# Kernel tuning notes

Hardware: AMD Instinct MI355X
Metric: run time of the kernel (lower is better)

## Reference

```python
import jax, jax.numpy as jnp
import numpy as np

N, P, S, M, K, L = 1024, 4, 12, 64, 16, 8
SNR = 20.0
PWR = 1.0
DECAY = L // 2  # Channel is built with decay = L // 2
MK = M + K
SMK = (S + 1) * MK
LOUT = L + SMK - 1  # full linear-convolution length


def _to_c(x):
    return x[..., 0] + 1j * x[..., 1]


def _to_r(x):
    return jnp.stack([x.real, x.imag], axis=-1)


def setup_inputs() -> dict:
    key = jax.random.key(0)
    k1, k2, k3, k4 = jax.random.split(key, 4)
    return {
        "x": jax.random.normal(k1, (N, P, S, M, 2), jnp.float32),
        "pilot_raw": jax.random.normal(k2, (N, P, 1, M, 2), jnp.float32),
        "cof_unit": jax.random.normal(k3, (N, P, L, 2), jnp.float32),
        "noise_unit": jax.random.normal(k4, (N, P, S + 1, MK, 2), jnp.float32),
    }


def reference(x, pilot_raw, cof_unit, noise_unit):
    # --- pilot: Normalize -> ifft -> add CP (done once in torch __init__) ---
    power = jnp.mean(pilot_raw ** 2, axis=(-2, -1), keepdims=True)  # (N,P,1,1,1)
    alpha = jnp.sqrt(PWR / 2) / jnp.sqrt(power)
    pilot = jnp.fft.ifft(_to_c(alpha * pilot_raw), axis=-1)          # (N,P,1,M) complex
    pilot = jnp.concatenate([pilot[..., -K:], pilot], axis=-1)        # add CP -> (N,P,1,MK)

    # --- payload: ifft -> add CP ---
    xt = jnp.fft.ifft(_to_c(x), axis=-1)                              # (N,P,S,M)
    xt = jnp.concatenate([xt[..., -K:], xt], axis=-1)                 # (N,P,S,MK)

    sig = jnp.concatenate([pilot, xt], axis=2).reshape(N, P, SMK)     # serialized complex signal

    # --- channel taps: sqrt(power_profile/2) * randn (cof is None path) ---
    prof = jnp.exp(-jnp.arange(L, dtype=jnp.float32) / DECAY)
    prof = prof / jnp.sum(prof)
    cof = _to_c(jnp.sqrt(prof / 2)[:, None] * cof_unit)               # (N,P,L) complex

    cof_true = jnp.concatenate([cof, jnp.zeros((N, P, M - L), cof.dtype)], axis=-1)
    H_true = jnp.fft.fft(cof_true, axis=-1)                           # (N,P,M)

    # --- L-tap linear convolution (equivalent to dense Toeplitz bmm) ---
    s_pad = jnp.pad(sig, ((0, 0), (0, 0), (L - 1, L - 1)))            # (N,P,SMK+2(L-1))
    y = jnp.zeros((N, P, LOUT), sig.dtype)
    for t in range(L):  # fixed small tap count
        y = y + cof[:, :, t:t + 1] * s_pad[:, :, L - 1 - t: L - 1 - t + LOUT]

    out = y[:, :, :SMK].reshape(N, P, S + 1, MK)

    # --- AWGN (default SNR path, isTest=False) ---
    noise_pwr = PWR / (M * 10.0 ** (0.1 * SNR))
    out = out + np.sqrt(noise_pwr / 2) * _to_c(noise_unit)

    # --- split pilot/signal, remove CP, FFT back to frequency domain ---
    info_pilot = jnp.fft.fft(out[:, :, 0:1, K:], axis=-1)             # (N,P,1,M)
    info_sig = jnp.fft.fft(out[:, :, 1:, K:], axis=-1)                # (N,P,S,M)

    return (_to_r(info_pilot), _to_r(info_sig), _to_r(H_true),
            jnp.float32(noise_pwr))
```

## Files before the change

kernel.cpp:

```cpp
#include <hip/hip_runtime.h>
#include <math.h>

#define NN   1024
#define PP   4
#define SS   12
#define MM   64
#define KK   16
#define LL   8
#define MKK  80
#define NSYM 13
#define SMK  1040
#define NITEMS 832

#define OFF_PILOT  0
#define OFF_SIG    524288
#define OFF_H      6815744
#define OFF_SCALAR 7340032

#define NOISE_PWR   1.5625e-4f
#define NOISE_SCALE 8.8388347648318447e-3f
#define TWO_SUM_PROF 7.8179726742f

__device__ __forceinline__ float2 shflx(float2 v, int mask) {
    return make_float2(__shfl_xor(v.x, mask), __shfl_xor(v.y, mask));
}

template<int DIR>
__device__ __forceinline__ float2 fft64(float2 v, const float2* tw, int lane) {
    #pragma unroll
    for (int s = 0; s < 6; ++s) {
        const int half = 32 >> s;
        float2 o = shflx(v, half);
        const bool up = (lane & half) != 0;
        float dx = up ? (o.x - v.x) : (o.x + v.x);
        float dy = up ? (o.y - v.y) : (o.y + v.y);
        float tx = tw[s].x;
        float ty = DIR ? -tw[s].y : tw[s].y;
        v.x = dx * tx - dy * ty;
        v.y = dx * ty + dy * tx;
    }
    return v;
}

__global__ __launch_bounds__(256) void ofdm_kernel(
    const float2* __restrict__ x,
    const float2* __restrict__ pilot_raw,
    const float2* __restrict__ cof_unit,
    const float2* __restrict__ noise_unit,
    float2* __restrict__ out_pilot,
    float2* __restrict__ out_sig,
    float2* __restrict__ out_H,
    float*  __restrict__ out_scalar)
{
    const int b    = blockIdx.x;
    const int tid  = threadIdx.x;
    const int wid  = tid >> 6;
    const int lane = tid & 63;

    __shared__ float2 sig[SMK];
    __shared__ float2 z[NITEMS];
    __shared__ float2 cofs[LL];

    const float2* xb = x          + (size_t)b * (SS*MM);
    const float2* pb = pilot_raw  + (size_t)b * MM;
    const float2* cb = cof_unit   + (size_t)b * LL;
    const float2* nb = noise_unit + (size_t)b * (NSYM*MKK);

    if (tid < LL) {
        float sc = sqrtf(__expf(-(float)tid * 0.25f) * (1.0f / TWO_SUM_PROF));
        float2 u = cb[tid];
        cofs[tid] = make_float2(sc * u.x, sc * u.y);
    }

    float2 twid[6];
    #pragma unroll
    for (int s = 0; s < 6; ++s) {
        const int half = 32 >> s;
        const int m = lane & (half - 1);
        float ang = -6.2831853071795864769f * (float)(m << s) * (1.0f / 64.0f);
        float sn, cs;
        __sincosf(ang, &sn, &cs);
        twid[s] = (lane & half) ? make_float2(cs, sn) : make_float2(1.0f, 0.0f);
    }

    const int rb = (int)(__brev((unsigned)lane) >> 26);

    float alpha = 0.0f;
    float2 pv = make_float2(0.f, 0.f);
    if (wid == 0) {
        pv = pb[lane];
        float ss = pv.x * pv.x + pv.y * pv.y;
        #pragma unroll
        for (int off = 32; off > 0; off >>= 1)
            ss += __shfl_xor(ss, off);
        alpha = sqrtf(64.0f / ss);
    }

    for (int sym = wid; sym < NSYM; sym += 4) {
        float2 v;
        if (sym == 0) v = make_float2(alpha * pv.x, alpha * pv.y);
        else          v = xb[(sym - 1) * MM + lane];
        v = fft64<1>(v, twid, lane);
        v.x *= (1.0f / 64.0f);
        v.y *= (1.0f / 64.0f);
        const int n = rb;
        sig[sym * MKK + KK + n] = v;
        if (n >= MM - KK) sig[sym * MKK + n - (MM - KK)] = v;
    }

    if (wid == 1) {
        float2 h = make_float2(0.f, 0.f);
        if (lane < LL) {
            float sc = sqrtf(__expf(-(float)lane * 0.25f) * (1.0f / TWO_SUM_PROF));
            float2 u = cb[lane];
            h = make_float2(sc * u.x, sc * u.y);
        }
        h = fft64<0>(h, twid, lane);
        out_H[(size_t)b * MM + rb] = h;
    }

    __syncthreads();

    for (int i = tid; i < NITEMS; i += 256) {
        const int s = i >> 6, m = i & 63;
        const int pos = s * MKK + KK + m;
        float2 acc = make_float2(0.f, 0.f);
        #pragma unroll
        for (int t = 0; t < LL; ++t) {
            float2 c = cofs[t];
            float2 v = sig[pos - t];
            acc.x += c.x * v.x - c.y * v.y;
            acc.y += c.x * v.y + c.y * v.x;
        }
        float2 nu = nb[pos];
        acc.x += NOISE_SCALE * nu.x;
        acc.y += NOISE_SCALE * nu.y;
        z[i] = acc;
    }

    __syncthreads();

    for (int sym = wid; sym < NSYM; sym += 4) {
        float2 v = z[sym * MM + lane];
        v = fft64<0>(v, twid, lane);
        if (sym == 0) out_pilot[(size_t)b * MM + rb] = v;
        else          out_sig[(size_t)b * (SS*MM) + (sym - 1) * MM + rb] = v;
    }

    if (b == 0 && tid == 0) out_scalar[0] = NOISE_PWR;
}

extern "C" void kernel_launch(void* const* d_in, const int* in_sizes, int n_in,
                              void* d_out, int out_size, void* d_ws, size_t ws_size,
                              hipStream_t stream) {
    const float2* x  = (const float2*)d_in[0];
    const float2* pr = (const float2*)d_in[1];
    const float2* cu = (const float2*)d_in[2];
    const float2* nu = (const float2*)d_in[3];

    float* out = (float*)d_out;
    float2* out_pilot = (float2*)(out + OFF_PILOT);
    float2* out_sig   = (float2*)(out + OFF_SIG);
    float2* out_H     = (float2*)(out + OFF_H);
    float*  out_sc    = out + OFF_SCALAR;

    ofdm_kernel<<<dim3(NN*PP), dim3(256), 0, stream>>>(
        x, pr, cu, nu, out_pilot, out_sig, out_H, out_sc);
}
```

Before: 127.8 us.

## Fuse FIR into bit-reversed-input DIT FFT and batch symbols per wavefront

Each wavefront now processes its three or four symbols at once, interleaving their shuffle-based FFTs to expose instruction-level parallelism. The forward FFT switches to decimation-in-time with bit-reversed input. This lets each lane compute the channel FIR plus noise directly at its bit-reversed position and feed it straight into the FFT, removing the z shared buffer and one __syncthreads. Channel taps are held in registers, and the H_true FFT is batched alongside the payload symbols. Outputs are now stored contiguously in natural order, at the cost of higher register pressure from the batched arrays.

After: 120.7 us. -5.5%, faster.

```diff
diff --git a/kernel.cpp b/kernel.cpp
--- a/kernel.cpp
+++ b/kernel.cpp
@@ -10,7 +10,6 @@
 #define MKK  80
 #define NSYM 13
 #define SMK  1040
-#define NITEMS 832
 
 #define OFF_PILOT  0
 #define OFF_SIG    524288
@@ -19,27 +18,52 @@
 
 #define NOISE_PWR   1.5625e-4f
 #define NOISE_SCALE 8.8388347648318447e-3f
-#define TWO_SUM_PROF 7.8179726742f
+#define INV_2SUM    0.1279105570f
 
 __device__ __forceinline__ float2 shflx(float2 v, int mask) {
     return make_float2(__shfl_xor(v.x, mask), __shfl_xor(v.y, mask));
 }
 
-template<int DIR>
-__device__ __forceinline__ float2 fft64(float2 v, const float2* tw, int lane) {
+
+template<int CONJ, int NS>
+__device__ __forceinline__ void fft64_dif(float2* v, const float2* tw, const float* sgn) {
+    #pragma unroll
+    for (int s = 5; s >= 0; --s) {
+        float2 o[NS];
+        #pragma unroll
+        for (int j = 0; j < NS; ++j) o[j] = shflx(v[j], 1 << s);
+        const float sg = sgn[s], tx = tw[s].x;
+        const float ty = CONJ ? -tw[s].y : tw[s].y;
+        #pragma unroll
+        for (int j = 0; j < NS; ++j) {
+            float dx = fmaf(sg, v[j].x, o[j].x);
+            float dy = fmaf(sg, v[j].y, o[j].y);
+            v[j].x = dx * tx - dy * ty;
+            v[j].y = dx * ty + dy * tx;
+        }
+    }
+}
+
+template<int NS>
+__device__ __forceinline__ void fft64_dit(float2* v, const float2* tw, const float* sgn) {
     #pragma unroll
     for (int s = 0; s < 6; ++s) {
-        const int half = 32 >> s;
-        float2 o = shflx(v, half);
-        const bool up = (lane & half) != 0;
-        float dx = up ? (o.x - v.x) : (o.x + v.x);
-        float dy = up ? (o.y - v.y) : (o.y + v.y);
-        float tx = tw[s].x;
-        float ty = DIR ? -tw[s].y : tw[s].y;
-        v.x = dx * tx - dy * ty;
-        v.y = dx * ty + dy * tx;
-    }
-    return v;
+        const float sg = sgn[s], tx = tw[s].x, ty = tw[s].y;
+        float ax[NS], ay[NS];
+        #pragma unroll
+        for (int j = 0; j < NS; ++j) {
+            ax[j] = v[j].x * tx - v[j].y * ty;
+            ay[j] = v[j].x * ty + v[j].y * tx;
+        }
+        float2 o[NS];
+        #pragma unroll
+        for (int j = 0; j < NS; ++j) o[j] = shflx(make_float2(ax[j], ay[j]), 1 << s);
+        #pragma unroll
+        for (int j = 0; j < NS; ++j) {
+            v[j].x = fmaf(sg, ax[j], o[j].x);
+            v[j].y = fmaf(sg, ay[j], o[j].y);
+        }
+    }
 }
 
 __global__ __launch_bounds__(256) void ofdm_kernel(
@@ -58,93 +82,120 @@
     const int lane = tid & 63;
 
     __shared__ float2 sig[SMK];
-    __shared__ float2 z[NITEMS];
-    __shared__ float2 cofs[LL];
 
     const float2* xb = x          + (size_t)b * (SS*MM);
     const float2* pb = pilot_raw  + (size_t)b * MM;
     const float2* cb = cof_unit   + (size_t)b * LL;
     const float2* nb = noise_unit + (size_t)b * (NSYM*MKK);
 
-    if (tid < LL) {
-        float sc = sqrtf(__expf(-(float)tid * 0.25f) * (1.0f / TWO_SUM_PROF));
-        float2 u = cb[tid];
-        cofs[tid] = make_float2(sc * u.x, sc * u.y);
-    }
-
-    float2 twid[6];
+    float2 tw[6];
+    float  sgn[6];
     #pragma unroll
     for (int s = 0; s < 6; ++s) {
-        const int half = 32 >> s;
-        const int m = lane & (half - 1);
-        float ang = -6.2831853071795864769f * (float)(m << s) * (1.0f / 64.0f);
+        const int h = 1 << s;
+        const bool up = (lane & h) != 0;
+        sgn[s] = up ? -1.0f : 1.0f;
+        float ang = -6.2831853071795864769f * (float)(lane & (h - 1)) / (float)(2 * h);
         float sn, cs;
         __sincosf(ang, &sn, &cs);
-        twid[s] = (lane & half) ? make_float2(cs, sn) : make_float2(1.0f, 0.0f);
-    }
-
+        tw[s] = up ? make_float2(cs, sn) : make_float2(1.0f, 0.0f);
+    }
     const int rb = (int)(__brev((unsigned)lane) >> 26);
 
-    float alpha = 0.0f;
-    float2 pv = make_float2(0.f, 0.f);
+    float2 cof[LL];
+    #pragma unroll
+    for (int t = 0; t < LL; ++t) {
+        float sc = sqrtf(__expf(-(float)t * 0.25f) * INV_2SUM);
+        float2 u = cb[t];
+        cof[t] = make_float2(sc * u.x, sc * u.y);
+    }
+
+    auto store_sig = [&](int sym, float2 vv) {
+        vv.x *= (1.0f / 64.0f);
+        vv.y *= (1.0f / 64.0f);
+        sig[sym * MKK + KK + rb] = vv;
+        if (rb >= MM - KK) sig[sym * MKK + rb - (MM - KK)] = vv;
+    };
+
     if (wid == 0) {
-        pv = pb[lane];
-        float ss = pv.x * pv.x + pv.y * pv.y;
+        float2 v[4];
+        float2 pv = pb[lane];
+        v[1] = xb[3 * MM + lane];
+        v[2] = xb[7 * MM + lane];
+        v[3] = xb[11 * MM + lane];
+        float ssq = pv.x * pv.x + pv.y * pv.y;
         #pragma unroll
         for (int off = 32; off > 0; off >>= 1)
-            ss += __shfl_xor(ss, off);
-        alpha = sqrtf(64.0f / ss);
-    }
-
-    for (int sym = wid; sym < NSYM; sym += 4) {
-        float2 v;
-        if (sym == 0) v = make_float2(alpha * pv.x, alpha * pv.y);
-        else          v = xb[(sym - 1) * MM + lane];
-        v = fft64<1>(v, twid, lane);
-        v.x *= (1.0f / 64.0f);
-        v.y *= (1.0f / 64.0f);
-        const int n = rb;
-        sig[sym * MKK + KK + n] = v;
-        if (n >= MM - KK) sig[sym * MKK + n - (MM - KK)] = v;
-    }
-
-    if (wid == 1) {
-        float2 h = make_float2(0.f, 0.f);
-        if (lane < LL) {
-            float sc = sqrtf(__expf(-(float)lane * 0.25f) * (1.0f / TWO_SUM_PROF));
-            float2 u = cb[lane];
-            h = make_float2(sc * u.x, sc * u.y);
-        }
-        h = fft64<0>(h, twid, lane);
-        out_H[(size_t)b * MM + rb] = h;
+            ssq += __shfl_xor(ssq, off);
+        float alpha = sqrtf(64.0f / ssq);
+        v[0] = make_float2(alpha * pv.x, alpha * pv.y);
+        fft64_dif<1, 4>(v, tw, sgn);
+        store_sig(0, v[0]); store_sig(4, v[1]); store_sig(8, v[2]); store_sig(12, v[3]);
+    } else {
+        float2 v[3];
+        v[0] = xb[(wid - 1) * MM + lane];
+        v[1] = xb[(wid + 3) * MM + lane];
+        v[2] = xb[(wid + 7) * MM + lane];
+        fft64_dif<1, 3>(v, tw, sgn);
+        store_sig(wid, v[0]); store_sig(wid + 4, v[1]); store_sig(wid + 8, v[2]);
     }
 
     __syncthreads();
 
-    for (int i = tid; i < NITEMS; i += 256) {
-        const int s = i >> 6, m = i & 63;
-        const int pos = s * MKK + KK + m;
-        float2 acc = make_float2(0.f, 0.f);
+    auto fir = [&](int sym) -> float2 {
+        const int pos = sym * MKK + KK + rb;
+        float2 nu = nb[pos];
+        float2 acc = make_float2(NOISE_SCALE * nu.x, NOISE_SCALE * nu.y);
         #pragma unroll
         for (int t = 0; t < LL; ++t) {
-            float2 c = cofs[t];
-            float2 v = sig[pos - t];
-            acc.x += c.x * v.x - c.y * v.y;
-            acc.y += c.x * v.y + c.y * v.x;
-        }
-        float2 nu = nb[pos];
-        acc.x += NOISE_SCALE * nu.x;
-        acc.y += NOISE_SCALE * nu.y;
-        z[i] = acc;
-    }
-
-    __syncthreads();
-
-    for (int sym = wid; sym < NSYM; sym += 4) {
-        float2 v = z[sym * MM + lane];
-        v = fft64<0>(v, twid, lane);
-        if (sym == 0) out_pilot[(size_t)b * MM + rb] = v;
-        else          out_sig[(size_t)b * (SS*MM) + (sym - 1) * MM + rb] = v;
+            float2 c = cof[t];
+            float2 s2 = sig[pos - t];
+            acc.x += c.x * s2.x - c.y * s2.y;
+            acc.y += c.x * s2.y + c.y * s2.x;
+        }
+        return acc;
+    };
+
+    const size_t ob = (size_t)b * MM;
+    const size_t osb = (size_t)b * (SS * MM);
+
+    if (wid <= 1) {
+        float2 v[4];
+        v[0] = fir(wid);
+        v[1] = fir(wid + 4);
+        v[2] = fir(wid + 8);
+        if (wid == 0) {
+            v[3] = fir(12);
+        } else {
+            float2 h = make_float2(0.0f, 0.0f);
+            if (rb < LL) {
+                float sc = sqrtf(__expf(-(float)rb * 0.25f) * INV_2SUM);
+                float2 u = cb[rb];
+                h = make_float2(sc * u.x, sc * u.y);
+            }
+            v[3] = h;
+        }
+        fft64_dit<4>(v, tw, sgn);
+        if (wid == 0) {
+            out_pilot[ob + lane]            = v[0];
+            out_sig[osb + 3 * MM + lane]    = v[1];
+            out_sig[osb + 7 * MM + lane]    = v[2];
+            out_sig[osb + 11 * MM + lane]   = v[3];
+        } else {
+            out_sig[osb + 0 * MM + lane]    = v[0];
+            out_sig[osb + 4 * MM + lane]    = v[1];
+            out_sig[osb + 8 * MM + lane]    = v[2];
+            out_H[ob + lane]                = v[3];
+        }
+    } else {
+        float2 v[3];
+        v[0] = fir(wid);
+        v[1] = fir(wid + 4);
+        v[2] = fir(wid + 8);
+        fft64_dit<3>(v, tw, sgn);
+        out_sig[osb + (wid - 1) * MM + lane] = v[0];
+        out_sig[osb + (wid + 3) * MM + lane] = v[1];
+        out_sig[osb + (wid + 7) * MM + lane] = v[2];
     }
 
     if (b == 0 && tid == 0) out_scalar[0] = NOISE_PWR;
```
